# Optimization experiments

Measured on AMD Instinct MI355X. Metric: run time of the kernel, lower is better.

## Reference

```python
import jax, jax.numpy as jnp
import numpy as np

N_NODES = 100000
N_EDGES = 3200000
N_GRAPHS = 512
IN_DIM = 29   # NUM_COMPONENT_TYPES(15) + NUM_PARAMS(14)
HID = 128
LAT = 256


def setup_inputs() -> dict:
    key = jax.random.key(0)
    ks = jax.random.split(key, 16)
    x = jax.random.normal(ks[0], (N_NODES, IN_DIM), dtype=jnp.float32)
    edge_index = jax.random.randint(ks[1], (2, N_EDGES), 0, N_NODES, dtype=jnp.int64)
    batch = jnp.sort(jax.random.randint(ks[2], (N_NODES,), 0, N_GRAPHS, dtype=jnp.int64))

    def lin(k, fan_in, fan_out):
        kw, kb = jax.random.split(k)
        s = 1.0 / np.sqrt(fan_in)
        W = jax.random.uniform(kw, (fan_in, fan_out), minval=-s, maxval=s, dtype=jnp.float32)
        b = jax.random.uniform(kb, (fan_out,), minval=-s, maxval=s, dtype=jnp.float32)
        return W, b

    W1, b1 = lin(ks[3], IN_DIM, HID)
    W2, b2 = lin(ks[4], HID, HID)
    W3, b3 = lin(ks[5], HID, HID)
    Wmu, bmu = lin(ks[6], HID, LAT)
    Wlv, blv = lin(ks[7], HID, LAT)
    return {"x": x, "edge_index": edge_index, "batch": batch,
            "W1": W1, "b1": b1, "W2": W2, "b2": b2, "W3": W3, "b3": b3,
            "Wmu": Wmu, "bmu": bmu, "Wlv": Wlv, "blv": blv}


def _gcn_conv(h, W, b, src, dst, dis):
    # PyG GCNConv: out = D^-1/2 (A + I) D^-1/2 (h W) + b
    hw = h @ W                                   # [N, out]
    norm = dis[src] * dis[dst]                   # [E]
    agg = jax.ops.segment_sum(hw[src] * norm[:, None], dst, num_segments=h.shape[0])
    return agg + hw * (dis * dis)[:, None] + b   # self-loop term has norm dis[i]^2


def reference(x, edge_index, batch, W1, b1, W2, b2, W3, b3, Wmu, bmu, Wlv, blv):
    src, dst = edge_index[0], edge_index[1]
    # symmetric degree with self-loops (computed once, identical across layers)
    deg = jax.ops.segment_sum(jnp.ones(src.shape[0], jnp.float32), dst,
                              num_segments=x.shape[0]) + 1.0
    dis = jax.lax.rsqrt(deg)

    h = jax.nn.relu(_gcn_conv(x, W1, b1, src, dst, dis))
    h = jax.nn.relu(_gcn_conv(h, W2, b2, src, dst, dis))
    h = jax.nn.relu(_gcn_conv(h, W3, b3, src, dst, dis))

    # global_mean_pool over graph ids
    sums = jax.ops.segment_sum(h, batch, num_segments=N_GRAPHS)
    cnts = jax.ops.segment_sum(jnp.ones(h.shape[0], jnp.float32), batch,
                               num_segments=N_GRAPHS)
    pooled = sums / jnp.maximum(cnts, 1.0)[:, None]   # [G, HID]

    mu = pooled @ Wmu + bmu
    logvar = pooled @ Wlv + blv
    return (mu, logvar)
```

## Files before the change

kernel.cpp:

```cpp
#include <hip/hip_runtime.h>
#include <hip/hip_bf16.h>

#define N_NODES 100000
#define N_EDGES 3200000
#define N_GRAPHS 512
#define IN_DIM 29
#define HID 128
#define LAT 256
#define NB 391
#define CAP 9216

typedef unsigned int uint;
typedef unsigned short ushort;
typedef float v4f __attribute__((ext_vector_type(4)));
typedef short v8s __attribute__((ext_vector_type(8)));

__device__ __forceinline__ ushort f2bf(float f) {
    uint u = __float_as_uint(f);
    return (ushort)((u + 0x7FFFu + ((u >> 16) & 1u)) >> 16);
}
__device__ __forceinline__ float bf2f(ushort h) { return __uint_as_float(((uint)h) << 16); }
__device__ __forceinline__ float bf_lo(uint p) { return __uint_as_float(p << 16); }
__device__ __forceinline__ float bf_hi(uint p) { return __uint_as_float(p & 0xFFFF0000u); }
__device__ __forceinline__ uint pack2(float a, float b) {
    return (uint)f2bf(a) | ((uint)f2bf(b) << 16);
}

__device__ __forceinline__ void bfadd(float* a, uint4 q) {
    a[0] += bf_lo(q.x); a[1] += bf_hi(q.x);
    a[2] += bf_lo(q.y); a[3] += bf_hi(q.y);
    a[4] += bf_lo(q.z); a[5] += bf_hi(q.z);
    a[6] += bf_lo(q.w); a[7] += bf_hi(q.w);
}

__device__ __forceinline__ v4f bf4(uint2 q) {
    return (v4f){bf_lo(q.x), bf_hi(q.x), bf_lo(q.y), bf_hi(q.y)};
}


__global__ __launch_bounds__(1024, 2) void k_binA(const int* __restrict__ src, const int* __restrict__ dst,
                                                  int* __restrict__ bktCnt, int* __restrict__ packed, int e) {
    __shared__ int hist[NB];
    __shared__ int base[NB];
    int t = threadIdx.x;
    for (int i = t; i < NB; i += 1024) hist[i] = 0;
    __syncthreads();
    int d[8], s[8];
    const int blockStart = blockIdx.x * 8192;
    #pragma unroll
    for (int k = 0; k < 8; ++k) {
        int idx = blockStart + k * 1024 + t;
        if (idx < e) {
            d[k] = dst[idx];
            s[k] = src[idx];
            atomicAdd(&hist[d[k] >> 8], 1);
        } else d[k] = -1;
    }
    __syncthreads();
    for (int i = t; i < NB; i += 1024) {
        int c = hist[i];
        base[i] = c ? atomicAdd(&bktCnt[i], c) : 0;
    }
    __syncthreads();
    #pragma unroll
    for (int k = 0; k < 8; ++k) {
        if (d[k] >= 0) {
            int b = d[k] >> 8;
            int pos = atomicAdd(&base[b], 1);
            if (pos < CAP) packed[b * CAP + pos] = ((d[k] & 255) << 17) | s[k];
        }
    }
}

__global__ __launch_bounds__(1024, 2) void k_binB(const int* __restrict__ bktCnt,
                                                  const int* __restrict__ packed, int* __restrict__ col,
                                                  int* __restrict__ rp, float* __restrict__ dis,
                                                  const float* __restrict__ x, ushort* __restrict__ xt16, int n) {
    __shared__ int cnt[8192];
    __shared__ int sh[1024];
    __shared__ float sdis[256];
    const int b = blockIdx.x;
    int cntB = bktCnt[b];
    if (cntB > CAP) cntB = CAP;
    const int segS = b * CAP;
    int t = threadIdx.x;
    int part = 0;
    for (int i = t; i < b; i += 1024) {
        int c = bktCnt[i];
        part += (c > CAP) ? CAP : c;
    }
    #pragma unroll
    for (int k = 0; k < 8; ++k) cnt[t + k * 1024] = 0;
    sh[t] = part;
    __syncthreads();
    for (int off = 512; off > 0; off >>= 1) {
        if (t < off) sh[t] += sh[t + off];
        __syncthreads();
    }
    const int colBase = sh[0];
    for (int j = t; j < cntB; j += 1024) {
        int pk = packed[segS + j];
        int key = ((pk >> 17) << 5) | ((pk & 0x1FFFF) >> 12);
        atomicAdd(&cnt[key], 1);
    }
    __syncthreads();
    int base8 = t << 3;
    int v[8];
    int sum = 0;
    #pragma unroll
    for (int k = 0; k < 8; ++k) { v[k] = cnt[base8 + k]; sum += v[k]; }
    sh[t] = sum;
    __syncthreads();
    for (int off = 1; off < 1024; off <<= 1) {
        int x2 = (t >= off) ? sh[t - off] : 0;
        __syncthreads();
        sh[t] += x2;
        __syncthreads();
    }
    int run = colBase + sh[t] - sum;
    #pragma unroll
    for (int k = 0; k < 8; ++k) { cnt[base8 + k] = run; run += v[k]; }
    __syncthreads();
    if (t < 256) {
        int node = (b << 8) + t;
        int start = cnt[t << 5];
        int next = (t == 255) ? (colBase + cntB) : cnt[(t + 1) << 5];
        int deg = next - start;
        float dv = rsqrtf((float)deg + 1.0f);
        sdis[t] = dv;
        if (node <= n) rp[node] = start;
        if (node < n) dis[node] = dv;
    }
    __syncthreads();
    for (int idx = t; idx < 256 * 32; idx += 1024) {
        int loc = idx >> 5;
        int node = (b << 8) + loc;
        if (node < n) {
            int k = idx & 31;
            float vv = (k < IN_DIM) ? x[(size_t)node * IN_DIM + k] * sdis[loc] : 0.f;
            xt16[((size_t)node << 5) + k] = f2bf(vv);
        }
    }
    for (int j = t; j < cntB; j += 1024) {
        int pk = packed[segS + j];
        int key = ((pk >> 17) << 5) | ((pk & 0x1FFFF) >> 12);
        int pos = atomicAdd(&cnt[key], 1);
        col[pos] = pk & 0x1FFFF;
    }
}


__device__ __forceinline__ void pack_one(const float* W, ushort* hi, ushort* lo, int Ksrc, int idx) {
    int j = idx & 7;
    int lane = (idx >> 3) & 63;
    int nt = (idx >> 9) & 7;
    int ks = idx >> 12;
    int k = ks * 32 + (lane >> 4) * 8 + j;
    int n = nt * 16 + (lane & 15);
    float v = (k < Ksrc) ? W[k * 128 + n] : 0.f;
    ushort h = f2bf(v);
    ushort l = f2bf(v - bf2f(h));
    hi[idx] = h;
    lo[idx] = l;
}

__global__ __launch_bounds__(256) void k_pack_all(const float* __restrict__ W1, const float* __restrict__ W2,
                                                  const float* __restrict__ W3,
                                                  ushort* w1h, ushort* w1l, ushort* w2h, ushort* w2l,
                                                  ushort* w3h, ushort* w3l, int* __restrict__ bktCnt,
                                                  float* __restrict__ pooled) {
    int idx = blockIdx.x * 256 + threadIdx.x;
    if (idx < NB) bktCnt[idx] = 0;
    if (idx < N_GRAPHS * HID) pooled[idx] = 0.f;
    if (idx < 4096) {
        pack_one(W1, w1h, w1l, IN_DIM, idx);
    } else if (idx < 4096 + 16384) {
        pack_one(W2, w2h, w2l, HID, idx - 4096);
    } else if (idx < 4096 + 32768) {
        pack_one(W3, w3h, w3l, HID, idx - 4096 - 16384);
    }
}


__global__ __launch_bounds__(256, 6) void k_l1(const ushort* __restrict__ xt16, const int* __restrict__ rp,
                                               const int* __restrict__ col, const float* __restrict__ dis,
                                               const ushort* __restrict__ Whi, const ushort* __restrict__ Wlo,
                                               const float* __restrict__ bias, ushort* __restrict__ out, int n) {
    __shared__ float yl[32][36];
    int t = threadIdx.x;
    int loc = t >> 3;
    int node = blockIdx.x * 32 + loc;
    int c4 = (t & 7) << 2;
    if (node < n) {
        int s = rp[node], e = rp[node + 1];
        v4f A = (v4f){0.f, 0.f, 0.f, 0.f};
        v4f B = (v4f){0.f, 0.f, 0.f, 0.f};
        int j = s;
        for (; j + 7 < e; j += 8) {
            int c0 = col[j],     c1 = col[j + 1], c2 = col[j + 2], c3 = col[j + 3];
            int c4i = col[j + 4], c5 = col[j + 5], c6 = col[j + 6], c7 = col[j + 7];
            uint2 q0 = *(const uint2*)(xt16 + ((size_t)c0 << 5) + c4);
            uint2 q1 = *(const uint2*)(xt16 + ((size_t)c1 << 5) + c4);
            uint2 q2 = *(const uint2*)(xt16 + ((size_t)c2 << 5) + c4);
            uint2 q3 = *(const uint2*)(xt16 + ((size_t)c3 << 5) + c4);
            uint2 q4 = *(const uint2*)(xt16 + ((size_t)c4i << 5) + c4);
            uint2 q5 = *(const uint2*)(xt16 + ((size_t)c5 << 5) + c4);
            uint2 q6 = *(const uint2*)(xt16 + ((size_t)c6 << 5) + c4);
            uint2 q7 = *(const uint2*)(xt16 + ((size_t)c7 << 5) + c4);
            A += bf4(q0); B += bf4(q1); A += bf4(q2); B += bf4(q3);
            A += bf4(q4); B += bf4(q5); A += bf4(q6); B += bf4(q7);
        }
        if (j + 3 < e) {
            int c0 = col[j], c1 = col[j + 1], c2 = col[j + 2], c3 = col[j + 3];
            uint2 q0 = *(const uint2*)(xt16 + ((size_t)c0 << 5) + c4);
            uint2 q1 = *(const uint2*)(xt16 + ((size_t)c1 << 5) + c4);
            uint2 q2 = *(const uint2*)(xt16 + ((size_t)c2 << 5) + c4);
            uint2 q3 = *(const uint2*)(xt16 + ((size_t)c3 << 5) + c4);
            A += bf4(q0); B += bf4(q1); A += bf4(q2); B += bf4(q3);
            j += 4;
        }
        for (; j < e; ++j) {
            int c = col[j];
            A += bf4(*(const uint2*)(xt16 + ((size_t)c << 5) + c4));
        }
        A += bf4(*(const uint2*)(xt16 + ((size_t)node << 5) + c4));
        float dv = dis[node];
        v4f o = (A + B) * dv;
        yl[loc][c4 + 0] = o.x;
        yl[loc][c4 + 1] = o.y;
        yl[loc][c4 + 2] = o.z;
        yl[loc][c4 + 3] = o.w;
    }
    __syncthreads();
    const int wave = t >> 6;
    const int lane = t & 63;
    const int mrow = ((wave >> 1) << 4) + (lane & 15);
    const int ntBase = (wave & 1) * 4;
    const int kh = (lane >> 4) * 8;
    float a[8];
    #pragma unroll
    for (int j = 0; j < 8; ++j) a[j] = yl[mrow][kh + j];
    v8s ahi, alo;
    #pragma unroll
    for (int j = 0; j < 8; ++j) {
        ushort h = f2bf(a[j]);
        ushort l = f2bf(a[j] - bf2f(h));
        ahi[j] = (short)h;
        alo[j] = (short)l;
    }
    const ushort* bh = Whi + (size_t)lane * 8;
    const ushort* bl = Wlo + (size_t)lane * 8;
    v4f acc[4];
    #pragma unroll
    for (int i = 0; i < 4; ++i) acc[i] = (v4f){0.f, 0.f, 0.f, 0.f};
    #pragma unroll
    for (int i = 0; i < 4; ++i) {
        int nt = ntBase + i;
        v8s bhi = *(const v8s*)(bh + nt * 512);
        v8s blo = *(const v8s*)(bl + nt * 512);
        acc[i] = __builtin_amdgcn_mfma_f32_16x16x32_bf16(ahi, bhi, acc[i], 0, 0, 0);
        acc[i] = __builtin_amdgcn_mfma_f32_16x16x32_bf16(ahi, blo, acc[i], 0, 0, 0);
        acc[i] = __builtin_amdgcn_mfma_f32_16x16x32_bf16(alo, bhi, acc[i], 0, 0, 0);
    }
    const int col0 = lane & 15;
    const int orow0 = blockIdx.x * 32 + ((wave >> 1) << 4) + ((lane >> 4) << 2);
    float bb[4];
    #pragma unroll
    for (int i = 0; i < 4; ++i) bb[i] = bias[(ntBase + i) * 16 + col0];
    #pragma unroll
    for (int r = 0; r < 4; ++r) {
        int orow = orow0 + r;
        if (orow < n) {
            #pragma unroll
            for (int i = 0; i < 4; ++i)
                out[(size_t)orow * 128 + (ntBase + i) * 16 + col0] = f2bf(fmaxf(acc[i][r] + bb[i], 0.f));
        }
    }
}


__global__ __launch_bounds__(256, 4) void k_gemm_bf32(const ushort* __restrict__ in,
                                                      const ushort* __restrict__ Whi,
                                                      const ushort* __restrict__ Wlo,
                                                      const float* __restrict__ dis,
                                                      ushort* __restrict__ out, int n) {
    const int wave = threadIdx.x >> 6;
    const int lane = threadIdx.x & 63;
    const int m0 = (blockIdx.x * 4 + wave) * 32;
    if (m0 >= n) return;
    int row0 = m0 + (lane & 15);
    int row1 = row0 + 16;
    if (row0 >= n) row0 = n - 1;
    if (row1 >= n) row1 = n - 1;
    const int kh = (lane >> 4) * 8;
    const ushort* rp0 = in + (size_t)row0 * 128 + kh;
    const ushort* rp1 = in + (size_t)row1 * 128 + kh;

    v4f acc0[8], acc1[8];
    #pragma unroll
    for (int t = 0; t < 8; ++t) {
        acc0[t] = (v4f){0.f, 0.f, 0.f, 0.f};
        acc1[t] = (v4f){0.f, 0.f, 0.f, 0.f};
    }

    #pragma unroll
    for (int ks = 0; ks < 4; ++ks) {
        v8s a0 = *(const v8s*)(rp0 + ks * 32);
        v8s a1 = *(const v8s*)(rp1 + ks * 32);
        const ushort* bh = Whi + (size_t)(ks * 8) * 512 + (size_t)lane * 8;
        const ushort* bl = Wlo + (size_t)(ks * 8) * 512 + (size_t)lane * 8;
        #pragma unroll
        for (int nt = 0; nt < 8; ++nt) {
            v8s bhi = *(const v8s*)(bh + nt * 512);
            v8s blo = *(const v8s*)(bl + nt * 512);
            acc0[nt] = __builtin_amdgcn_mfma_f32_16x16x32_bf16(a0, bhi, acc0[nt], 0, 0, 0);
            acc0[nt] = __builtin_amdgcn_mfma_f32_16x16x32_bf16(a0, blo, acc0[nt], 0, 0, 0);
            acc1[nt] = __builtin_amdgcn_mfma_f32_16x16x32_bf16(a1, bhi, acc1[nt], 0, 0, 0);
            acc1[nt] = __builtin_amdgcn_mfma_f32_16x16x32_bf16(a1, blo, acc1[nt], 0, 0, 0);
        }
    }

    const int col0 = lane & 15;
    const int orow0 = m0 + (lane >> 4) * 4;
    #pragma unroll
    for (int r = 0; r < 4; ++r) {
        int orow = orow0 + r;
        if (orow < n) {
            float dv = dis[orow];
            #pragma unroll
            for (int nt = 0; nt < 8; ++nt)
                out[(size_t)orow * 128 + nt * 16 + col0] = f2bf(acc0[nt][r] * dv);
        }
        int orow2 = orow + 16;
        if (orow2 < n) {
            float dv = dis[orow2];
            #pragma unroll
            for (int nt = 0; nt < 8; ++nt)
                out[(size_t)orow2 * 128 + nt * 16 + col0] = f2bf(acc1[nt][r] * dv);
        }
    }
}


__global__ __launch_bounds__(256, 6) void k_agg(const ushort* __restrict__ hws, const int* __restrict__ rp,
                                                const int* __restrict__ col, const float* __restrict__ dis,
                                                const float* __restrict__ bias, ushort* __restrict__ out, int n) {
    int g = blockIdx.x * 32 + (threadIdx.x >> 3);
    int node = (g < n) ? g : g - n;
    if (g >= 2 * n) return;
    int c8 = ((g < n) ? 0 : 64) + ((threadIdx.x & 7) << 3);
    int s = rp[node], e = rp[node + 1];
    float A[8] = {0.f, 0.f, 0.f, 0.f, 0.f, 0.f, 0.f, 0.f};
    float B[8] = {0.f, 0.f, 0.f, 0.f, 0.f, 0.f, 0.f, 0.f};
    int j = s;
    for (; j + 7 < e; j += 8) {
        int c0 = col[j],     c1 = col[j + 1], c2 = col[j + 2], c3 = col[j + 3];
        int c4 = col[j + 4], c5 = col[j + 5], c6 = col[j + 6], c7 = col[j + 7];
        uint4 q0 = *(const uint4*)(hws + ((size_t)c0 << 7) + c8);
        uint4 q1 = *(const uint4*)(hws + ((size_t)c1 << 7) + c8);
        uint4 q2 = *(const uint4*)(hws + ((size_t)c2 << 7) + c8);
        uint4 q3 = *(const uint4*)(hws + ((size_t)c3 << 7) + c8);
        uint4 q4 = *(const uint4*)(hws + ((size_t)c4 << 7) + c8);
        uint4 q5 = *(const uint4*)(hws + ((size_t)c5 << 7) + c8);
        uint4 q6 = *(const uint4*)(hws + ((size_t)c6 << 7) + c8);
        uint4 q7 = *(const uint4*)(hws + ((size_t)c7 << 7) + c8);
        bfadd(A, q0); bfadd(B, q1); bfadd(A, q2); bfadd(B, q3);
        bfadd(A, q4); bfadd(B, q5); bfadd(A, q6); bfadd(B, q7);
    }
    if (j + 3 < e) {
        int c0 = col[j], c1 = col[j + 1], c2 = col[j + 2], c3 = col[j + 3];
        uint4 q0 = *(const uint4*)(hws + ((size_t)c0 << 7) + c8);
        uint4 q1 = *(const uint4*)(hws + ((size_t)c1 << 7) + c8);
        uint4 q2 = *(const uint4*)(hws + ((size_t)c2 << 7) + c8);
        uint4 q3 = *(const uint4*)(hws + ((size_t)c3 << 7) + c8);
        bfadd(A, q0); bfadd(B, q1); bfadd(A, q2); bfadd(B, q3);
        j += 4;
    }
    for (; j < e; ++j) {
        int c = col[j];
        uint4 q = *(const uint4*)(hws + ((size_t)c << 7) + c8);
        bfadd(A, q);
    }
    uint4 qs = *(const uint4*)(hws + ((size_t)node << 7) + c8);
    bfadd(A, qs);
    float dv = dis[node];
    float4 bv0 = *(const float4*)(bias + c8);
    float4 bv1 = *(const float4*)(bias + c8 + 4);
    float r0 = fmaxf(dv * (A[0] + B[0]) + bv0.x, 0.f);
    float r1 = fmaxf(dv * (A[1] + B[1]) + bv0.y, 0.f);
    float r2 = fmaxf(dv * (A[2] + B[2]) + bv0.z, 0.f);
    float r3 = fmaxf(dv * (A[3] + B[3]) + bv0.w, 0.f);
    float r4 = fmaxf(dv * (A[4] + B[4]) + bv1.x, 0.f);
    float r5 = fmaxf(dv * (A[5] + B[5]) + bv1.y, 0.f);
    float r6 = fmaxf(dv * (A[6] + B[6]) + bv1.z, 0.f);
    float r7 = fmaxf(dv * (A[7] + B[7]) + bv1.w, 0.f);
    uint4 o;
    o.x = pack2(r0, r1);
    o.y = pack2(r2, r3);
    o.z = pack2(r4, r5);
    o.w = pack2(r6, r7);
    *(uint4*)(out + (size_t)node * 128 + c8) = o;
}


__global__ __launch_bounds__(256, 6) void k_agg_pool(const ushort* __restrict__ hws, const int* __restrict__ rp,
                                                     const int* __restrict__ col, const float* __restrict__ dis,
                                                     const float* __restrict__ bias, const int* __restrict__ batch,
                                                     float* __restrict__ pooled, int n) {
    __shared__ float red[256][8];
    __shared__ int gID[32];
    int t = threadIdx.x;
    int g = blockIdx.x * 32 + (t >> 3);
    int node = (g < n) ? g : g - n;
    int half = (g < n) ? 0 : 1;
    int c8 = half * 64 + ((t & 7) << 3);
    int s = rp[node], e = rp[node + 1];
    float A[8] = {0.f, 0.f, 0.f, 0.f, 0.f, 0.f, 0.f, 0.f};
    float B[8] = {0.f, 0.f, 0.f, 0.f, 0.f, 0.f, 0.f, 0.f};
    int j = s;
    for (; j + 7 < e; j += 8) {
        int c0 = col[j],     c1 = col[j + 1], c2 = col[j + 2], c3 = col[j + 3];
        int c4 = col[j + 4], c5 = col[j + 5], c6 = col[j + 6], c7 = col[j + 7];
        uint4 q0 = *(const uint4*)(hws + ((size_t)c0 << 7) + c8);
        uint4 q1 = *(const uint4*)(hws + ((size_t)c1 << 7) + c8);
        uint4 q2 = *(const uint4*)(hws + ((size_t)c2 << 7) + c8);
        uint4 q3 = *(const uint4*)(hws + ((size_t)c3 << 7) + c8);
        uint4 q4 = *(const uint4*)(hws + ((size_t)c4 << 7) + c8);
        uint4 q5 = *(const uint4*)(hws + ((size_t)c5 << 7) + c8);
        uint4 q6 = *(const uint4*)(hws + ((size_t)c6 << 7) + c8);
        uint4 q7 = *(const uint4*)(hws + ((size_t)c7 << 7) + c8);
        bfadd(A, q0); bfadd(B, q1); bfadd(A, q2); bfadd(B, q3);
        bfadd(A, q4); bfadd(B, q5); bfadd(A, q6); bfadd(B, q7);
    }
    if (j + 3 < e) {
        int c0 = col[j], c1 = col[j + 1], c2 = col[j + 2], c3 = col[j + 3];
        uint4 q0 = *(const uint4*)(hws + ((size_t)c0 << 7) + c8);
        uint4 q1 = *(const uint4*)(hws + ((size_t)c1 << 7) + c8);
        uint4 q2 = *(const uint4*)(hws + ((size_t)c2 << 7) + c8);
        uint4 q3 = *(const uint4*)(hws + ((size_t)c3 << 7) + c8);
        bfadd(A, q0); bfadd(B, q1); bfadd(A, q2); bfadd(B, q3);
        j += 4;
    }
    for (; j < e; ++j) {
        int c = col[j];
        uint4 q = *(const uint4*)(hws + ((size_t)c << 7) + c8);
        bfadd(A, q);
    }
    uint4 qs = *(const uint4*)(hws + ((size_t)node << 7) + c8);
    bfadd(A, qs);
    float dv = dis[node];
    float4 bv0 = *(const float4*)(bias + c8);
    float4 bv1 = *(const float4*)(bias + c8 + 4);
    red[t][0] = fmaxf(dv * (A[0] + B[0]) + bv0.x, 0.f);
    red[t][1] = fmaxf(dv * (A[1] + B[1]) + bv0.y, 0.f);
    red[t][2] = fmaxf(dv * (A[2] + B[2]) + bv0.z, 0.f);
    red[t][3] = fmaxf(dv * (A[3] + B[3]) + bv0.w, 0.f);
    red[t][4] = fmaxf(dv * (A[4] + B[4]) + bv1.x, 0.f);
    red[t][5] = fmaxf(dv * (A[5] + B[5]) + bv1.y, 0.f);
    red[t][6] = fmaxf(dv * (A[6] + B[6]) + bv1.z, 0.f);
    red[t][7] = fmaxf(dv * (A[7] + B[7]) + bv1.w, 0.f);
    if ((t & 7) == 0) gID[t >> 3] = batch[node];
    __syncthreads();
    if (t < 64) {
        int lane8 = t >> 3, k = t & 7;
        int g0 = gID[0], g1 = gID[31];
        float s0 = 0.f, s1 = 0.f;
        #pragma unroll 4
        for (int gr = 0; gr < 32; ++gr) {
            float v = red[(gr << 3) + lane8][k];
            if (gID[gr] == g0) s0 += v; else s1 += v;
        }
        int ch = half * 64 + (lane8 << 3) + k;
        atomicAdd(&pooled[(size_t)g0 * 128 + ch], s0);
        if (g1 != g0) atomicAdd(&pooled[(size_t)g1 * 128 + ch], s1);
    }
}


__global__ __launch_bounds__(256) void k_pool_head(const float* __restrict__ pooled, const int* __restrict__ batch,
                                                   const float* __restrict__ Wmu, const float* __restrict__ bmu,
                                                   const float* __restrict__ Wlv, const float* __restrict__ blv,
                                                   float* __restrict__ out, int n) {
    int g = blockIdx.x;
    int t = threadIdx.x;
    int lo = 0, hi = n;
    while (lo < hi) { int m = (lo + hi) >> 1; if (batch[m] < g) lo = m + 1; else hi = m; }
    int start = lo;
    hi = n;
    while (lo < hi) { int m = (lo + hi) >> 1; if (batch[m] < g + 1) lo = m + 1; else hi = m; }
    int end = lo;

    __shared__ float pl[128];
    float inv = 1.0f / fmaxf((float)(end - start), 1.0f);
    if (t < 128) pl[t] = pooled[(size_t)g * 128 + t] * inv;
    __syncthreads();
    float amu = bmu[t], alv = blv[t];
    for (int k = 0; k < 128; k += 4) {
        float p0 = pl[k], p1 = pl[k + 1], p2 = pl[k + 2], p3 = pl[k + 3];
        amu += p0 * Wmu[(k + 0) * 256 + t] + p1 * Wmu[(k + 1) * 256 + t]
             + p2 * Wmu[(k + 2) * 256 + t] + p3 * Wmu[(k + 3) * 256 + t];
        alv += p0 * Wlv[(k + 0) * 256 + t] + p1 * Wlv[(k + 1) * 256 + t]
             + p2 * Wlv[(k + 2) * 256 + t] + p3 * Wlv[(k + 3) * 256 + t];
    }
    out[(size_t)g * 256 + t] = amu;
    out[(size_t)N_GRAPHS * 256 + (size_t)g * 256 + t] = alv;
}


extern "C" void kernel_launch(void* const* d_in, const int* in_sizes, int n_in,
                              void* d_out, int out_size, void* d_ws, size_t ws_size,
                              hipStream_t stream) {
    const float* x    = (const float*)d_in[0];
    const int*   eidx = (const int*)d_in[1];
    const int*   batch= (const int*)d_in[2];
    const float* W1   = (const float*)d_in[3];
    const float* b1   = (const float*)d_in[4];
    const float* W2   = (const float*)d_in[5];
    const float* b2   = (const float*)d_in[6];
    const float* W3   = (const float*)d_in[7];
    const float* b3   = (const float*)d_in[8];
    const float* Wmu  = (const float*)d_in[9];
    const float* bmu  = (const float*)d_in[10];
    const float* Wlv  = (const float*)d_in[11];
    const float* blv  = (const float*)d_in[12];
    float* out = (float*)d_out;

    const int N = N_NODES, E = N_EDGES;
    const int* srcp = eidx;
    const int* dstp = eidx + E;

    ushort* w1h = (ushort*)d_ws;
    ushort* w1l = w1h + 4096;
    ushort* w2h = w1l + 4096;
    ushort* w2l = w2h + 16384;
    ushort* w3h = w2l + 16384;
    ushort* w3l = w3h + 16384;
    ushort* A   = w3l + 16384;
    ushort* B   = A + (size_t)N * 128;
    float*  dis = (float*)(B + (size_t)N * 128);
    int*   rp   = (int*)(dis + N);
    int*   bktCnt   = rp + (N + 2);
    int*   colStart = bktCnt + 512;
    int*   packed = colStart + 512;
    int*   col    = packed + (size_t)NB * CAP;
    float* pooled = (float*)(col + (size_t)E);

    ushort* xt16 = A;

    const int gE8192 = (E + 8191) / 8192;

    k_pack_all<<<256, 256, 0, stream>>>(W1, W2, W3, w1h, w1l, w2h, w2l, w3h, w3l, bktCnt, pooled);

    k_binA<<<gE8192, 1024, 0, stream>>>(srcp, dstp, bktCnt, packed, E);
    k_binB<<<NB, 1024, 0, stream>>>(bktCnt, packed, col, rp, dis, x, xt16, N);

    const int gGemm2 = (N + 127) / 128;
    const int gL1    = (N + 31) / 32;
    const int gAgg   = (2 * N + 31) / 32;

    k_l1<<<gL1, 256, 0, stream>>>(xt16, rp, col, dis, w1h, w1l, b1, B, N);

    k_gemm_bf32<<<gGemm2, 256, 0, stream>>>(B, w2h, w2l, dis, A, N);
    k_agg<<<gAgg, 256, 0, stream>>>(A, rp, col, dis, b2, B, N);
    k_gemm_bf32<<<gGemm2, 256, 0, stream>>>(B, w3h, w3l, dis, A, N);
    k_agg_pool<<<gAgg, 256, 0, stream>>>(A, rp, col, dis, b3, batch, pooled, N);
    k_pool_head<<<N_GRAPHS, 256, 0, stream>>>(pooled, batch, Wmu, bmu, Wlv, blv, out, N);
}
```

Baseline: 432.3 us.

## Balance layer-1 edge gather across threads and use wave-shuffle scans in binning

In the layer-1 kernel each block's edge range is now split evenly across 32 thread slots, each covering a contiguous chunk that may span node boundaries. Partial sums are flushed into shared memory with atomic adds, replacing one thread group per node, which left threads idle on uneven degrees. The binning kernel's shared-memory block reduction and Hillis-Steele scan are replaced with wave shuffles plus a small per-wave scan, cutting the number of barriers. The costs are LDS atomics, a binary search per slot, and the unrolled 8-way loads giving way to a simpler per-edge loop. The self-loop path also drops the node<n guard, so the last partial block relies on padding.

```diff
diff --git a/kernel.cpp b/kernel.cpp
--- a/kernel.cpp
+++ b/kernel.cpp
@@ -77,27 +77,28 @@
                                                   int* __restrict__ rp, float* __restrict__ dis,
                                                   const float* __restrict__ x, ushort* __restrict__ xt16, int n) {
     __shared__ int cnt[8192];
-    __shared__ int sh[1024];
+    __shared__ int wsum[16];
     __shared__ float sdis[256];
     const int b = blockIdx.x;
     int cntB = bktCnt[b];
     if (cntB > CAP) cntB = CAP;
     const int segS = b * CAP;
     int t = threadIdx.x;
+    int lane = t & 63, wid = t >> 6;
     int part = 0;
     for (int i = t; i < b; i += 1024) {
         int c = bktCnt[i];
         part += (c > CAP) ? CAP : c;
     }
     #pragma unroll
+    for (int d = 1; d < 64; d <<= 1) part += __shfl_xor(part, d, 64);
+    if (lane == 0) wsum[wid] = part;
+    #pragma unroll
     for (int k = 0; k < 8; ++k) cnt[t + k * 1024] = 0;
-    sh[t] = part;
-    __syncthreads();
-    for (int off = 512; off > 0; off >>= 1) {
-        if (t < off) sh[t] += sh[t + off];
-        __syncthreads();
-    }
-    const int colBase = sh[0];
+    __syncthreads();
+    int colBase = 0;
+    #pragma unroll
+    for (int w = 0; w < 16; ++w) colBase += wsum[w];
     for (int j = t; j < cntB; j += 1024) {
         int pk = packed[segS + j];
         int key = ((pk >> 17) << 5) | ((pk & 0x1FFFF) >> 12);
@@ -109,15 +110,26 @@
     int sum = 0;
     #pragma unroll
     for (int k = 0; k < 8; ++k) { v[k] = cnt[base8 + k]; sum += v[k]; }
-    sh[t] = sum;
-    __syncthreads();
-    for (int off = 1; off < 1024; off <<= 1) {
-        int x2 = (t >= off) ? sh[t - off] : 0;
-        __syncthreads();
-        sh[t] += x2;
-        __syncthreads();
-    }
-    int run = colBase + sh[t] - sum;
+    int inc = sum;
+    #pragma unroll
+    for (int d = 1; d < 64; d <<= 1) {
+        int nv = __shfl_up(inc, d, 64);
+        if (lane >= d) inc += nv;
+    }
+    if (lane == 63) wsum[wid] = inc;
+    __syncthreads();
+    if (t < 16) {
+        int wv = wsum[t];
+        int winc = wv;
+        #pragma unroll
+        for (int d = 1; d < 16; d <<= 1) {
+            int nv = __shfl_up(winc, d, 16);
+            if ((t & 15) >= d) winc += nv;
+        }
+        wsum[t] = winc - wv;
+    }
+    __syncthreads();
+    int run = colBase + wsum[wid] + (inc - sum);
     #pragma unroll
     for (int k = 0; k < 8; ++k) { cnt[base8 + k] = run; run += v[k]; }
     __syncthreads();
@@ -187,49 +199,56 @@
                                                const ushort* __restrict__ Whi, const ushort* __restrict__ Wlo,
                                                const float* __restrict__ bias, ushort* __restrict__ out, int n) {
     __shared__ float yl[32][36];
+    __shared__ int rpl[33];
     int t = threadIdx.x;
-    int loc = t >> 3;
-    int node = blockIdx.x * 32 + loc;
-    int c4 = (t & 7) << 2;
-    if (node < n) {
-        int s = rp[node], e = rp[node + 1];
-        v4f A = (v4f){0.f, 0.f, 0.f, 0.f};
-        v4f B = (v4f){0.f, 0.f, 0.f, 0.f};
-        int j = s;
-        for (; j + 7 < e; j += 8) {
-            int c0 = col[j],     c1 = col[j + 1], c2 = col[j + 2], c3 = col[j + 3];
-            int c4i = col[j + 4], c5 = col[j + 5], c6 = col[j + 6], c7 = col[j + 7];
-            uint2 q0 = *(const uint2*)(xt16 + ((size_t)c0 << 5) + c4);
-            uint2 q1 = *(const uint2*)(xt16 + ((size_t)c1 << 5) + c4);
-            uint2 q2 = *(const uint2*)(xt16 + ((size_t)c2 << 5) + c4);
-            uint2 q3 = *(const uint2*)(xt16 + ((size_t)c3 << 5) + c4);
-            uint2 q4 = *(const uint2*)(xt16 + ((size_t)c4i << 5) + c4);
-            uint2 q5 = *(const uint2*)(xt16 + ((size_t)c5 << 5) + c4);
-            uint2 q6 = *(const uint2*)(xt16 + ((size_t)c6 << 5) + c4);
-            uint2 q7 = *(const uint2*)(xt16 + ((size_t)c7 << 5) + c4);
-            A += bf4(q0); B += bf4(q1); A += bf4(q2); B += bf4(q3);
-            A += bf4(q4); B += bf4(q5); A += bf4(q6); B += bf4(q7);
-        }
-        if (j + 3 < e) {
-            int c0 = col[j], c1 = col[j + 1], c2 = col[j + 2], c3 = col[j + 3];
-            uint2 q0 = *(const uint2*)(xt16 + ((size_t)c0 << 5) + c4);
-            uint2 q1 = *(const uint2*)(xt16 + ((size_t)c1 << 5) + c4);
-            uint2 q2 = *(const uint2*)(xt16 + ((size_t)c2 << 5) + c4);
-            uint2 q3 = *(const uint2*)(xt16 + ((size_t)c3 << 5) + c4);
-            A += bf4(q0); B += bf4(q1); A += bf4(q2); B += bf4(q3);
-            j += 4;
-        }
-        for (; j < e; ++j) {
+    const int base = blockIdx.x * 32;
+    if (t < 33) rpl[t] = rp[base + t];
+    for (int i = t; i < 32 * 32; i += 256) yl[i >> 5][i & 31] = 0.f;
+    __syncthreads();
+    const int e0 = rpl[0], e1 = rpl[32];
+    const int cnt = e1 - e0;
+    const int slot = t >> 3;
+    const int ch4 = (t & 7) << 2;
+    const int chunk = (cnt + 31) >> 5;
+    int jb = e0 + slot * chunk;
+    int je = jb + chunk;
+    if (je > e1) je = e1;
+    if (jb < je) {
+        int lo = 0, hi = 32;
+        while (lo + 1 < hi) { int m = (lo + hi) >> 1; if (rpl[m] <= jb) lo = m; else hi = m; }
+        int nodeEnd = rpl[lo + 1];
+        v4f acc = (v4f){0.f, 0.f, 0.f, 0.f};
+        #pragma unroll 4
+        for (int j = jb; j < je; ++j) {
+            while (j >= nodeEnd) {
+                atomicAdd(&yl[lo][ch4 + 0], acc.x);
+                atomicAdd(&yl[lo][ch4 + 1], acc.y);
+                atomicAdd(&yl[lo][ch4 + 2], acc.z);
+                atomicAdd(&yl[lo][ch4 + 3], acc.w);
+                acc = (v4f){0.f, 0.f, 0.f, 0.f};
+                ++lo;
+                nodeEnd = rpl[lo + 1];
+            }
             int c = col[j];
-            A += bf4(*(const uint2*)(xt16 + ((size_t)c << 5) + c4));
-        }
-        A += bf4(*(const uint2*)(xt16 + ((size_t)node << 5) + c4));
+            acc += bf4(*(const uint2*)(xt16 + ((size_t)c << 5) + ch4));
+        }
+        atomicAdd(&yl[lo][ch4 + 0], acc.x);
+        atomicAdd(&yl[lo][ch4 + 1], acc.y);
+        atomicAdd(&yl[lo][ch4 + 2], acc.z);
+        atomicAdd(&yl[lo][ch4 + 3], acc.w);
+    }
+    __syncthreads();
+    {
+        int loc = t >> 3, c4 = (t & 7) << 2;
+        int node = base + loc;
+        v4f self = bf4(*(const uint2*)(xt16 + ((size_t)node << 5) + c4));
         float dv = dis[node];
-        v4f o = (A + B) * dv;
-        yl[loc][c4 + 0] = o.x;
-        yl[loc][c4 + 1] = o.y;
-        yl[loc][c4 + 2] = o.z;
-        yl[loc][c4 + 3] = o.w;
+        v4f sum = (v4f){yl[loc][c4], yl[loc][c4 + 1], yl[loc][c4 + 2], yl[loc][c4 + 3]};
+        sum = (sum + self) * dv;
+        yl[loc][c4 + 0] = sum.x;
+        yl[loc][c4 + 1] = sum.y;
+        yl[loc][c4 + 2] = sum.z;
+        yl[loc][c4 + 3] = sum.w;
     }
     __syncthreads();
     const int wave = t >> 6;
@@ -250,17 +269,17 @@
     }
     const ushort* bh = Whi + (size_t)lane * 8;
     const ushort* bl = Wlo + (size_t)lane * 8;
-    v4f acc[4];
-    #pragma unroll
-    for (int i = 0; i < 4; ++i) acc[i] = (v4f){0.f, 0.f, 0.f, 0.f};
+    v4f acc2[4];
+    #pragma unroll
+    for (int i = 0; i < 4; ++i) acc2[i] = (v4f){0.f, 0.f, 0.f, 0.f};
     #pragma unroll
     for (int i = 0; i < 4; ++i) {
         int nt = ntBase + i;
         v8s bhi = *(const v8s*)(bh + nt * 512);
         v8s blo = *(const v8s*)(bl + nt * 512);
-        acc[i] = __builtin_amdgcn_mfma_f32_16x16x32_bf16(ahi, bhi, acc[i], 0, 0, 0);
-        acc[i] = __builtin_amdgcn_mfma_f32_16x16x32_bf16(ahi, blo, acc[i], 0, 0, 0);
-        acc[i] = __builtin_amdgcn_mfma_f32_16x16x32_bf16(alo, bhi, acc[i], 0, 0, 0);
+        acc2[i] = __builtin_amdgcn_mfma_f32_16x16x32_bf16(ahi, bhi, acc2[i], 0, 0, 0);
+        acc2[i] = __builtin_amdgcn_mfma_f32_16x16x32_bf16(ahi, blo, acc2[i], 0, 0, 0);
+        acc2[i] = __builtin_amdgcn_mfma_f32_16x16x32_bf16(alo, bhi, acc2[i], 0, 0, 0);
     }
     const int col0 = lane & 15;
     const int orow0 = blockIdx.x * 32 + ((wave >> 1) << 4) + ((lane >> 4) << 2);
@@ -273,7 +292,7 @@
         if (orow < n) {
             #pragma unroll
             for (int i = 0; i < 4; ++i)
-                out[(size_t)orow * 128 + (ntBase + i) * 16 + col0] = f2bf(fmaxf(acc[i][r] + bb[i], 0.f));
+                out[(size_t)orow * 128 + (ntBase + i) * 16 + col0] = f2bf(fmaxf(acc2[i][r] + bb[i], 0.f));
         }
     }
 }
```

Measured after the change: 464.7 us. 7.5% more time.
